# Performance work log

Hardware: AMD Instinct MI355X
Metric: run time of the kernel (lower is better)

The kernel has to match this reference:

```python
import jax, jax.numpy as jnp
import numpy as np

B, S, D, H, G = 4, 2048, 1024, 16, 32
HD = D // H
LN_EPS = 1e-5


def _lin_init(key, fan_in, fan_out):
    kw, kb = jax.random.split(key)
    bound = 1.0 / np.sqrt(fan_in)
    W = jax.random.uniform(kw, (fan_in, fan_out), jnp.float32, -bound, bound)
    b = jax.random.uniform(kb, (fan_out,), jnp.float32, -bound, bound)
    return W, b


def setup_inputs() -> dict:
    key = jax.random.key(0)
    ks = jax.random.split(key, 9)
    x = jax.random.normal(ks[0], (B, S, D), jnp.float32)
    geo_features = jax.random.normal(ks[1], (B, G), jnp.float32)
    Wq, bq = _lin_init(ks[2], D, D)
    Wk, bk = _lin_init(ks[3], D, D)
    Wv, bv = _lin_init(ks[4], D, D)
    Wo, bo = _lin_init(ks[5], D, D)
    ge_W1, ge_b1 = _lin_init(ks[6], G, D)
    ln_g = jnp.ones((D,), jnp.float32)
    ln_b = jnp.zeros((D,), jnp.float32)
    ge_W2, ge_b2 = _lin_init(ks[7], D, D)
    gm_W, gm_b = _lin_init(ks[8], D, H)
    return dict(x=x, geo_features=geo_features, Wq=Wq, bq=bq, Wk=Wk, bk=bk,
                Wv=Wv, bv=bv, Wo=Wo, bo=bo, ge_W1=ge_W1, ge_b1=ge_b1,
                ln_g=ln_g, ln_b=ln_b, ge_W2=ge_W2, ge_b2=ge_b2,
                gm_W=gm_W, gm_b=gm_b)


def reference(x, geo_features, Wq, bq, Wk, bk, Wv, bv, Wo, bo,
              ge_W1, ge_b1, ln_g, ln_b, ge_W2, ge_b2, gm_W, gm_b):
    # QKV projections -> (B, H, S, HD)
    def split_heads(t):
        return t.reshape(B, S, H, HD).transpose(0, 2, 1, 3)
    Q = split_heads(x @ Wq + bq)
    K = split_heads(x @ Wk + bk)
    V = split_heads(x @ Wv + bv)

    # geo encoder: Linear -> LayerNorm -> ReLU -> Linear
    h = geo_features @ ge_W1 + ge_b1                      # (B, D)
    mu = jnp.mean(h, axis=-1, keepdims=True)
    var = jnp.mean(jnp.square(h - mu), axis=-1, keepdims=True)
    h = (h - mu) / jnp.sqrt(var + LN_EPS) * ln_g + ln_b
    h = jax.nn.relu(h)
    geo_encoded = h @ ge_W2 + ge_b2                       # (B, D)
    geo_mod = jax.nn.sigmoid(geo_encoded @ gm_W + gm_b)   # (B, H)

    scale = 1.0 / np.sqrt(HD)
    scores = jnp.einsum('bhqd,bhkd->bhqk', Q, K) * scale  # (B, H, S, S)
    scores = scores * (1.0 + geo_mod[:, :, None, None])
    attn = jax.nn.softmax(scores, axis=-1)                # dropout in eval mode: identity
    ctx = jnp.einsum('bhqk,bhkd->bhqd', attn, V)          # (B, H, S, HD)
    ctx = ctx.transpose(0, 2, 1, 3).reshape(B, S, D)
    out = ctx @ Wo + bo
    return out, attn
```

## Files before the change

### kernel.cpp

```cpp
#include <hip/hip_runtime.h>

typedef __attribute__((ext_vector_type(8))) short bf16x8;
typedef __attribute__((ext_vector_type(4))) float f32x4;
typedef __attribute__((ext_vector_type(4))) unsigned short us4;
typedef unsigned short u16;

#define MB (1024*1024)

__device__ __forceinline__ u16 f2bf(float f) {
    unsigned u = __float_as_uint(f);
    unsigned r = (u + 0x7fffu + ((u >> 16) & 1u)) >> 16;
    return (u16)r;
}

__device__ __forceinline__ f32x4 mfma16(bf16x8 a, bf16x8 b, f32x4 c) {
    return __builtin_amdgcn_mfma_f32_16x16x32_bf16(a, b, c, 0, 0, 0);
}

__device__ __forceinline__ void gload16(const void* g, void* l) {
    __builtin_amdgcn_global_load_lds(
        (__attribute__((address_space(1))) void*)(unsigned long long)g,
        (__attribute__((address_space(3))) void*)l, 16, 0, 0);
}

__global__ __launch_bounds__(256) void k_cvtx(const float* __restrict__ x, u16* __restrict__ xb) {
    const long long i = (long long)blockIdx.x * 256 + threadIdx.x;
    const float4* xp = (const float4*)x;
    float4 a = xp[i*2], b = xp[i*2+1];
    bf16x8 o;
    o[0]=(short)f2bf(a.x); o[1]=(short)f2bf(a.y); o[2]=(short)f2bf(a.z); o[3]=(short)f2bf(a.w);
    o[4]=(short)f2bf(b.x); o[5]=(short)f2bf(b.y); o[6]=(short)f2bf(b.z); o[7]=(short)f2bf(b.w);
    *(bf16x8*)&xb[i*8] = o;
}

__global__ __launch_bounds__(256) void k_wtcvt(const float* __restrict__ W0, const float* __restrict__ W1,
                                               const float* __restrict__ W2, const float* __restrict__ W3,
                                               u16* __restrict__ wt) {
    __shared__ float tl[32][33];
    const int t = threadIdx.x, z = blockIdx.z;
    const float* W = (z==0)?W0:(z==1)?W1:(z==2)?W2:W3;
    const int k0 = blockIdx.x*32, n0 = blockIdx.y*32;
    const int r = t >> 3, c4 = (t & 7) * 4;
    float4 v = *(const float4*)&W[(long long)(k0+r)*1024 + n0 + c4];
    tl[r][c4] = v.x; tl[r][c4+1] = v.y; tl[r][c4+2] = v.z; tl[r][c4+3] = v.w;
    __syncthreads();
    us4 ov;
    ov[0] = f2bf(tl[c4+0][r]); ov[1] = f2bf(tl[c4+1][r]);
    ov[2] = f2bf(tl[c4+2][r]); ov[3] = f2bf(tl[c4+3][r]);
    *(us4*)&wt[((long long)z << 20) + (long long)(n0+r)*1024 + k0 + c4] = ov;
}

__global__ __launch_bounds__(1024) void k_geo1(const float* __restrict__ geo, const float* __restrict__ W1,
                                               const float* __restrict__ b1, const float* __restrict__ lng,
                                               const float* __restrict__ lnb, float* __restrict__ hr) {
    const int b = blockIdx.x, j = threadIdx.x;
    float acc = b1[j];
    #pragma unroll 8
    for (int g = 0; g < 32; ++g) acc += geo[b*32+g] * W1[(long long)g*1024 + j];
    float s1 = acc, s2 = acc*acc;
    #pragma unroll
    for (int m = 1; m < 64; m <<= 1) { s1 += __shfl_xor(s1, m); s2 += __shfl_xor(s2, m); }
    __shared__ float r1[16], r2[16];
    __shared__ float mu_s, rv_s;
    const int wid = threadIdx.x >> 6, lid = threadIdx.x & 63;
    if (lid == 0) { r1[wid] = s1; r2[wid] = s2; }
    __syncthreads();
    if (threadIdx.x == 0) {
        float S1 = 0.f, S2 = 0.f;
        for (int i = 0; i < 16; ++i) { S1 += r1[i]; S2 += r2[i]; }
        float mu = S1 / 1024.f;
        float var = S2 / 1024.f - mu*mu;
        mu_s = mu; rv_s = rsqrtf(var + 1e-5f);
    }
    __syncthreads();
    float hv = (acc - mu_s) * rv_s * lng[j] + lnb[j];
    hr[b*1024 + j] = fmaxf(hv, 0.f);
}

__global__ __launch_bounds__(256) void k_geo2(const float* __restrict__ hr, const float* __restrict__ W2,
                                              const float* __restrict__ b2, float* __restrict__ ge) {
    const int b = blockIdx.x >> 2;
    const int j = (blockIdx.x & 3)*256 + threadIdx.x;
    __shared__ float hs[1024];
    #pragma unroll
    for (int i = 0; i < 4; ++i) hs[threadIdx.x*4 + i] = hr[b*1024 + threadIdx.x*4 + i];
    __syncthreads();
    float acc = b2[j];
    #pragma unroll 8
    for (int d = 0; d < 1024; ++d) acc += hs[d] * W2[(long long)d*1024 + j];
    ge[b*1024 + j] = acc;
}

__global__ __launch_bounds__(64) void k_geo3(const float* __restrict__ ge, const float* __restrict__ gmW,
                                             const float* __restrict__ gmb, float* __restrict__ qs) {
    const int t = threadIdx.x;
    const int b = t >> 4, hh = t & 15;
    float acc = gmb[hh];
    #pragma unroll 8
    for (int d = 0; d < 1024; ++d) acc += ge[b*1024 + d] * gmW[d*16 + hh];
    qs[t] = 0.125f * (1.f + 1.f/(1.f + __expf(-acc)));
}

__global__ __launch_bounds__(256) void k_qkv_gemm(const u16* __restrict__ xb, const u16* __restrict__ wtq,
                                                  const float* __restrict__ bq, const float* __restrict__ bk,
                                                  const float* __restrict__ bv, u16* __restrict__ outq) {
    __shared__ u16 lA[128*64];
    __shared__ u16 lB[128*64];
    const int t = threadIdx.x, z = blockIdx.z;
    const int m0 = blockIdx.y * 128, n0 = blockIdx.x * 128;
    const u16* wt = wtq + (long long)z * (1024*1024);
    const float* bias = (z==0) ? bq : (z==1) ? bk : bv;
    u16* out = outq + (long long)z * 8388608;
    const int w = t >> 6, l = t & 63, lm = l & 15, lg = l >> 4;
    const int wr = (w >> 1) * 64, wc = (w & 1) * 64;
    f32x4 acc[4][4] = {};
    const char* gA = (const char*)xb + (long long)(m0 + (t>>3))*2048 + (t&7)*16;
    const char* gB = (const char*)wt + (long long)(n0 + (t>>3))*2048 + (t&7)*16;
    char* lAp = (char*)lA + t*16;
    char* lBp = (char*)lB + t*16;
    for (int k0 = 0; k0 < 1024; k0 += 64) {
        #pragma unroll
        for (int i = 0; i < 4; ++i) {
            gload16(gA + (long long)i*32*2048, lAp + i*4096);
            gload16(gB + (long long)i*32*2048, lBp + i*4096);
        }
        gA += 128; gB += 128;
        __syncthreads();
        #pragma unroll
        for (int kk = 0; kk < 2; ++kk) {
            bf16x8 af[4], bfr[4];
            #pragma unroll
            for (int mi = 0; mi < 4; ++mi)
                af[mi] = *(const bf16x8*)((const char*)lA + (wr + mi*16 + lm)*128 + kk*64 + lg*16);
            #pragma unroll
            for (int ni = 0; ni < 4; ++ni)
                bfr[ni] = *(const bf16x8*)((const char*)lB + (wc + ni*16 + lm)*128 + kk*64 + lg*16);
            #pragma unroll
            for (int mi = 0; mi < 4; ++mi)
                #pragma unroll
                for (int ni = 0; ni < 4; ++ni)
                    acc[mi][ni] = mfma16(af[mi], bfr[ni], acc[mi][ni]);
        }
        __syncthreads();
    }
    #pragma unroll
    for (int ni = 0; ni < 4; ++ni) {
        const int n = n0 + wc + ni*16 + lm;
        const float bn = bias[n];
        const int hh = n >> 6, d = n & 63;
        #pragma unroll
        for (int mi = 0; mi < 4; ++mi) {
            #pragma unroll
            for (int r = 0; r < 4; ++r) {
                const int m = m0 + wr + mi*16 + lg*4 + r;
                const int b = m >> 11, s = m & 2047;
                out[(((long long)b*16 + hh)*2048 + s)*64 + d] = f2bf(acc[mi][ni][r] + bn);
            }
        }
    }
}

__global__ __launch_bounds__(256) void k_vtrans(const u16* __restrict__ vb, u16* __restrict__ vt) {
    __shared__ u16 tl[64][40];
    const int t = threadIdx.x;
    const int bh = blockIdx.z, s0 = blockIdx.y*64, d0 = blockIdx.x*32;
    const u16* vsrc = vb + (long long)bh*2048*64;
    {
        const int sl = t >> 2, dg = t & 3;
        bf16x8 v = *(const bf16x8*)&vsrc[(long long)(s0+sl)*64 + d0 + dg*8];
        *(bf16x8*)&tl[sl][dg*8] = v;
    }
    __syncthreads();
    {
        const int dl = t >> 3, sg = t & 7;
        bf16x8 o;
        #pragma unroll
        for (int j = 0; j < 8; ++j) o[j] = (short)tl[sg*8+j][dl];
        *(bf16x8*)&vt[((long long)bh*64 + d0+dl)*2048 + s0 + sg*8] = o;
    }
}

__global__ __launch_bounds__(256) void k_attn(const u16* __restrict__ Qb, const u16* __restrict__ Kb,
                                              const u16* __restrict__ Vt, const float* __restrict__ qsv,
                                              float* __restrict__ attn_out, u16* __restrict__ ctxb) {
    __shared__ u16 lK[128*64];
    __shared__ u16 lV[64*128];
    __shared__ u16 lP[128*128];

    const int nl = blockIdx.x;
    const int ob = (nl & 7)*128 + (nl >> 3);
    const int bh = ob >> 4, qt = ob & 15;
    const int t = threadIdx.x, w = t >> 6, l = t & 63, lm = l & 15, lg = l >> 4;
    const int q0 = qt * 128;
    const float qs = qsv[bh];

    const char* KB = (const char*)Kb + (long long)bh * (2048*64*2);
    const char* VB = (const char*)Vt + (long long)bh * (2048*64*2);

    bf16x8 qf[2][2];
    {
        const char* QB = (const char*)Qb + (long long)bh * (2048*64*2);
        #pragma unroll
        for (int ms = 0; ms < 2; ++ms)
            #pragma unroll
            for (int kc = 0; kc < 2; ++kc)
                qf[ms][kc] = *(const bf16x8*)(QB + (long long)(q0 + w*32 + ms*16 + lm)*128 + kc*64 + lg*16);
    }

    int koff[4], voff[4], loff[4];
    #pragma unroll
    for (int i = 0; i < 4; ++i) {
        int off = i*4096 + t*16;
        loff[i] = off;
        int rowk = off >> 7, pck = off & 127;
        koff[i] = rowk*128 + (pck ^ ((rowk & 7) << 4));
        int rowv = off >> 8, pcv = off & 255;
        voff[i] = rowv*4096 + (pcv ^ ((rowv & 7) << 4));
    }

    float lsum[2][4] = {};
    for (int kt = 0; kt < 16; ++kt) {
        #pragma unroll
        for (int i = 0; i < 4; ++i)
            gload16(KB + kt*16384 + koff[i], (char*)lK + loff[i]);
        __syncthreads();
        #pragma unroll
        for (int ns = 0; ns < 8; ++ns) {
            const int rowb = ns*16 + lm;
            const int tag = (rowb & 7) << 4;
            bf16x8 kf0 = *(const bf16x8*)((const char*)lK + rowb*128 + ((lg*16) ^ tag));
            bf16x8 kf1 = *(const bf16x8*)((const char*)lK + rowb*128 + ((64 + lg*16) ^ tag));
            #pragma unroll
            for (int ms = 0; ms < 2; ++ms) {
                f32x4 acc = {};
                acc = mfma16(qf[ms][0], kf0, acc);
                acc = mfma16(qf[ms][1], kf1, acc);
                #pragma unroll
                for (int r = 0; r < 4; ++r)
                    lsum[ms][r] += __expf(acc[r] * qs);
            }
        }
        __syncthreads();
    }
    float invl[2][4];
    #pragma unroll
    for (int ms = 0; ms < 2; ++ms)
        #pragma unroll
        for (int r = 0; r < 4; ++r) {
            float v = lsum[ms][r];
            v += __shfl_xor(v, 1); v += __shfl_xor(v, 2);
            v += __shfl_xor(v, 4); v += __shfl_xor(v, 8);
            invl[ms][r] = 1.f / v;
        }

    f32x4 cacc[2][4] = {};
    float* aout = attn_out + (long long)bh*2048*2048 + (long long)(q0 + w*32)*2048;
    for (int kt = 0; kt < 16; ++kt) {
        #pragma unroll
        for (int i = 0; i < 4; ++i)
            gload16(KB + kt*16384 + koff[i], (char*)lK + loff[i]);
        #pragma unroll
        for (int i = 0; i < 4; ++i)
            gload16(VB + kt*256 + voff[i], (char*)lV + loff[i]);
        __syncthreads();

        #pragma unroll
        for (int ns = 0; ns < 8; ++ns) {
            const int rowb = ns*16 + lm;
            const int tag = (rowb & 7) << 4;
            bf16x8 kf0 = *(const bf16x8*)((const char*)lK + rowb*128 + ((lg*16) ^ tag));
            bf16x8 kf1 = *(const bf16x8*)((const char*)lK + rowb*128 + ((64 + lg*16) ^ tag));
            #pragma unroll
            for (int ms = 0; ms < 2; ++ms) {
                f32x4 acc = {};
                acc = mfma16(qf[ms][0], kf0, acc);
                acc = mfma16(qf[ms][1], kf1, acc);
                #pragma unroll
                for (int r = 0; r < 4; ++r) {
                    const float p = __expf(acc[r]*qs) * invl[ms][r];
                    const int row = ms*16 + lg*4 + r;
                    __builtin_nontemporal_store(p, &aout[(long long)row*2048 + kt*128 + ns*16 + lm]);
                    const int prow = w*32 + row;
                    *(u16*)((char*)lP + prow*256 + (((ns*16 + lm)*2) ^ ((prow & 7) << 4))) = f2bf(p);
                }
            }
        }
        #pragma unroll
        for (int ks = 0; ks < 4; ++ks) {
            bf16x8 pa[2];
            #pragma unroll
            for (int ms = 0; ms < 2; ++ms) {
                const int prow = w*32 + ms*16 + lm;
                pa[ms] = *(const bf16x8*)((const char*)lP + prow*256 + ((ks*64 + lg*16) ^ ((prow & 7) << 4)));
            }
            #pragma unroll
            for (int dn = 0; dn < 4; ++dn) {
                const int rowv = dn*16 + lm;
                bf16x8 vf = *(const bf16x8*)((const char*)lV + rowv*256 + ((ks*64 + lg*16) ^ ((rowv & 7) << 4)));
                cacc[0][dn] = mfma16(pa[0], vf, cacc[0][dn]);
                cacc[1][dn] = mfma16(pa[1], vf, cacc[1][dn]);
            }
        }
        __syncthreads();
    }

    const int b = bh >> 4, hh = bh & 15;
    #pragma unroll
    for (int ms = 0; ms < 2; ++ms)
        #pragma unroll
        for (int dn = 0; dn < 4; ++dn)
            #pragma unroll
            for (int r = 0; r < 4; ++r) {
                const int q = q0 + w*32 + ms*16 + lg*4 + r;
                ctxb[(((long long)b*2048 + q)*16 + hh)*64 + dn*16 + lm] = f2bf(cacc[ms][dn][r]);
            }
}

__global__ __launch_bounds__(256) void k_o_gemm(const u16* __restrict__ ab, const u16* __restrict__ wt,
                                                const float* __restrict__ bo, float* __restrict__ outf) {
    __shared__ u16 lA[128*64];
    __shared__ u16 lB[128*64];
    const int t = threadIdx.x;
    const int m0 = blockIdx.y * 128, n0 = blockIdx.x * 128;
    const int w = t >> 6, l = t & 63, lm = l & 15, lg = l >> 4;
    const int wr = (w >> 1) * 64, wc = (w & 1) * 64;
    f32x4 acc[4][4] = {};
    const char* gA = (const char*)ab + (long long)(m0 + (t>>3))*2048 + (t&7)*16;
    const char* gB = (const char*)wt + (long long)(n0 + (t>>3))*2048 + (t&7)*16;
    char* lAp = (char*)lA + t*16;
    char* lBp = (char*)lB + t*16;
    for (int k0 = 0; k0 < 1024; k0 += 64) {
        #pragma unroll
        for (int i = 0; i < 4; ++i) {
            gload16(gA + (long long)i*32*2048, lAp + i*4096);
            gload16(gB + (long long)i*32*2048, lBp + i*4096);
        }
        gA += 128; gB += 128;
        __syncthreads();
        #pragma unroll
        for (int kk = 0; kk < 2; ++kk) {
            bf16x8 af[4], bfr[4];
            #pragma unroll
            for (int mi = 0; mi < 4; ++mi)
                af[mi] = *(const bf16x8*)((const char*)lA + (wr + mi*16 + lm)*128 + kk*64 + lg*16);
            #pragma unroll
            for (int ni = 0; ni < 4; ++ni)
                bfr[ni] = *(const bf16x8*)((const char*)lB + (wc + ni*16 + lm)*128 + kk*64 + lg*16);
            #pragma unroll
            for (int mi = 0; mi < 4; ++mi)
                #pragma unroll
                for (int ni = 0; ni < 4; ++ni)
                    acc[mi][ni] = mfma16(af[mi], bfr[ni], acc[mi][ni]);
        }
        __syncthreads();
    }
    #pragma unroll
    for (int ni = 0; ni < 4; ++ni) {
        const int n = n0 + wc + ni*16 + lm;
        const float bn = bo[n];
        #pragma unroll
        for (int mi = 0; mi < 4; ++mi) {
            #pragma unroll
            for (int r = 0; r < 4; ++r) {
                const int m = m0 + wr + mi*16 + lg*4 + r;
                outf[(long long)m*1024 + n] = acc[mi][ni][r] + bn;
            }
        }
    }
}

extern "C" void kernel_launch(void* const* d_in, const int* in_sizes, int n_in,
                              void* d_out, int out_size, void* d_ws, size_t ws_size,
                              hipStream_t stream) {
    const float* x    = (const float*)d_in[0];
    const float* geo  = (const float*)d_in[1];
    const float* Wq   = (const float*)d_in[2];
    const float* bq   = (const float*)d_in[3];
    const float* Wk   = (const float*)d_in[4];
    const float* bk   = (const float*)d_in[5];
    const float* Wv   = (const float*)d_in[6];
    const float* bv   = (const float*)d_in[7];
    const float* Wo   = (const float*)d_in[8];
    const float* bo   = (const float*)d_in[9];
    const float* geW1 = (const float*)d_in[10];
    const float* geb1 = (const float*)d_in[11];
    const float* lng  = (const float*)d_in[12];
    const float* lnb  = (const float*)d_in[13];
    const float* geW2 = (const float*)d_in[14];
    const float* geb2 = (const float*)d_in[15];
    const float* gmW  = (const float*)d_in[16];
    const float* gmb  = (const float*)d_in[17];

    char* ws = (char*)d_ws;
    u16* xb   = (u16*)(ws + 0);
    u16* wt   = (u16*)(ws + 16*(size_t)MB);
    u16* qkv  = (u16*)(ws + 24*(size_t)MB);
    u16* Qb   = qkv;
    u16* Kb   = (u16*)(ws + 40*(size_t)MB);
    u16* Vb   = (u16*)(ws + 56*(size_t)MB);
    u16* Vt   = (u16*)(ws + 72*(size_t)MB);
    u16* ctx  = Vb;
    float* hr = (float*)(ws + 88*(size_t)MB);
    float* ge = (float*)(ws + 88*(size_t)MB + 65536);
    float* qsb= (float*)(ws + 88*(size_t)MB + 131072);

    float* outf = (float*)d_out;
    float* attn = outf + 8388608;

    hipLaunchKernelGGL(k_cvtx,    dim3(4096),      dim3(256),  0, stream, x, xb);
    hipLaunchKernelGGL(k_wtcvt,   dim3(32,32,4),   dim3(256),  0, stream, Wq, Wk, Wv, Wo, wt);
    hipLaunchKernelGGL(k_geo1,    dim3(4),         dim3(1024), 0, stream, geo, geW1, geb1, lng, lnb, hr);
    hipLaunchKernelGGL(k_geo2,    dim3(16),        dim3(256),  0, stream, hr, geW2, geb2, ge);
    hipLaunchKernelGGL(k_geo3,    dim3(1),         dim3(64),   0, stream, ge, gmW, gmb, qsb);
    hipLaunchKernelGGL(k_qkv_gemm,dim3(8,64,3),    dim3(256),  0, stream, xb, wt, bq, bk, bv, qkv);
    hipLaunchKernelGGL(k_vtrans,  dim3(2,32,64),   dim3(256),  0, stream, Vb, Vt);
    hipLaunchKernelGGL(k_attn,    dim3(1024),      dim3(256),  0, stream, Qb, Kb, Vt, qsb, attn, ctx);
    hipLaunchKernelGGL(k_o_gemm,  dim3(8,64),      dim3(256),  0, stream, ctx, wt + 3*1048576, bo, outf);
}
```

Before: 572.0 us.

## Software-pipeline attention K/V loads with multi-buffered LDS and vectorized attn stores

Rewrites the attention kernel's two passes to use smaller 64-key tiles held in multiple LDS buffers: triple-buffered in the row-sum pass, double-buffered K and V in the output pass. The next tile's global loads are issued before the current tile's compute, with explicit vmcnt waits and barriers, so load latency can overlap MFMA work. The MFMA operands are swapped so each lane holds four consecutive keys for one query row. This allows 16-byte nontemporal stores of attention probabilities and packed bf16 conversion into the P tile. It also sets occupancy to three blocks per CU with a single 48KB LDS array. The hand-written waitcnt counts and barrier placement are fragile and could cause races if the counts are wrong.

```diff
diff --git a/kernel.cpp b/kernel.cpp
--- a/kernel.cpp
+++ b/kernel.cpp
@@ -7,10 +7,21 @@
 
 #define MB (1024*1024)
 
+#define WAITV(N) asm volatile("s_waitcnt vmcnt(" #N ")" ::: "memory")
+#define WAITL0() asm volatile("s_waitcnt lgkmcnt(0)" ::: "memory")
+#define BAR()    __builtin_amdgcn_s_barrier()
+#define SCHEDB() __builtin_amdgcn_sched_barrier(0)
+
 __device__ __forceinline__ u16 f2bf(float f) {
     unsigned u = __float_as_uint(f);
     unsigned r = (u + 0x7fffu + ((u >> 16) & 1u)) >> 16;
     return (u16)r;
+}
+
+__device__ __forceinline__ unsigned cvtpk(float a, float b) {
+    unsigned r;
+    asm("v_cvt_pk_bf16_f32 %0, %1, %2" : "=v"(r) : "v"(a), "v"(b));
+    return r;
 }
 
 __device__ __forceinline__ f32x4 mfma16(bf16x8 a, bf16x8 b, f32x4 c) {
@@ -180,12 +191,10 @@
     }
 }
 
-__global__ __launch_bounds__(256) void k_attn(const u16* __restrict__ Qb, const u16* __restrict__ Kb,
-                                              const u16* __restrict__ Vt, const float* __restrict__ qsv,
-                                              float* __restrict__ attn_out, u16* __restrict__ ctxb) {
-    __shared__ u16 lK[128*64];
-    __shared__ u16 lV[64*128];
-    __shared__ u16 lP[128*128];
+__global__ __launch_bounds__(256, 3) void k_attn(const u16* __restrict__ Qb, const u16* __restrict__ Kb,
+                                                 const u16* __restrict__ Vt, const float* __restrict__ qsv,
+                                                 float* __restrict__ attn_out, u16* __restrict__ ctxb) {
+    __shared__ char lds[49152];
 
     const int nl = blockIdx.x;
     const int ob = (nl & 7)*128 + (nl >> 3);
@@ -194,12 +203,12 @@
     const int q0 = qt * 128;
     const float qs = qsv[bh];
 
-    const char* KB = (const char*)Kb + (long long)bh * (2048*64*2);
-    const char* VB = (const char*)Vt + (long long)bh * (2048*64*2);
+    const char* KB = (const char*)Kb + (long long)bh * 262144;
+    const char* VB = (const char*)Vt + (long long)bh * 262144;
 
     bf16x8 qf[2][2];
     {
-        const char* QB = (const char*)Qb + (long long)bh * (2048*64*2);
+        const char* QB = (const char*)Qb + (long long)bh * 262144;
         #pragma unroll
         for (int ms = 0; ms < 2; ++ms)
             #pragma unroll
@@ -207,101 +216,139 @@
                 qf[ms][kc] = *(const bf16x8*)(QB + (long long)(q0 + w*32 + ms*16 + lm)*128 + kc*64 + lg*16);
     }
 
-    int koff[4], voff[4], loff[4];
-    #pragma unroll
-    for (int i = 0; i < 4; ++i) {
-        int off = i*4096 + t*16;
-        loff[i] = off;
-        int rowk = off >> 7, pck = off & 127;
-        koff[i] = rowk*128 + (pck ^ ((rowk & 7) << 4));
-        int rowv = off >> 8, pcv = off & 255;
-        voff[i] = rowv*4096 + (pcv ^ ((rowv & 7) << 4));
-    }
-
-    float lsum[2][4] = {};
-    for (int kt = 0; kt < 16; ++kt) {
-        #pragma unroll
-        for (int i = 0; i < 4; ++i)
-            gload16(KB + kt*16384 + koff[i], (char*)lK + loff[i]);
-        __syncthreads();
-        #pragma unroll
-        for (int ns = 0; ns < 8; ++ns) {
-            const int rowb = ns*16 + lm;
-            const int tag = (rowb & 7) << 4;
-            bf16x8 kf0 = *(const bf16x8*)((const char*)lK + rowb*128 + ((lg*16) ^ tag));
-            bf16x8 kf1 = *(const bf16x8*)((const char*)lK + rowb*128 + ((64 + lg*16) ^ tag));
-            #pragma unroll
-            for (int ms = 0; ms < 2; ++ms) {
-                f32x4 acc = {};
-                acc = mfma16(qf[ms][0], kf0, acc);
-                acc = mfma16(qf[ms][1], kf1, acc);
-                #pragma unroll
-                for (int r = 0; r < 4; ++r)
-                    lsum[ms][r] += __expf(acc[r] * qs);
-            }
-        }
-        __syncthreads();
-    }
-    float invl[2][4];
-    #pragma unroll
-    for (int ms = 0; ms < 2; ++ms)
-        #pragma unroll
-        for (int r = 0; r < 4; ++r) {
-            float v = lsum[ms][r];
-            v += __shfl_xor(v, 1); v += __shfl_xor(v, 2);
-            v += __shfl_xor(v, 4); v += __shfl_xor(v, 8);
-            invl[ms][r] = 1.f / v;
-        }
-
+    int offA[2], srcK[2], srcV[2];
+    #pragma unroll
+    for (int i = 0; i < 2; ++i) {
+        const int off = i*4096 + t*16;
+        const int row = off >> 7, cb = off & 127;
+        offA[i] = off;
+        srcK[i] = row*128  + (cb ^ ((row & 7) << 4));
+        srcV[i] = row*4096 + (cb ^ ((row & 7) << 4));
+    }
+
+    float lsum[2] = {0.f, 0.f};
+    {
+        #pragma unroll
+        for (int i = 0; i < 2; ++i) gload16(KB + srcK[i], lds + offA[i]);
+        #pragma unroll
+        for (int i = 0; i < 2; ++i) gload16(KB + 8192 + srcK[i], lds + 8192 + offA[i]);
+        SCHEDB();
+        WAITV(2); BAR(); SCHEDB();
+
+        int cb_ = 0, sb_ = 2;
+        for (int kt = 0; kt < 32; ++kt) {
+            const int ktn = (kt < 30) ? kt + 2 : 31;
+            {
+                char* dst = lds + sb_*8192;
+                #pragma unroll
+                for (int i = 0; i < 2; ++i)
+                    gload16(KB + (long long)ktn*8192 + srcK[i], dst + offA[i]);
+            }
+            SCHEDB();
+            const char* kb = lds + cb_*8192;
+            #pragma unroll
+            for (int ns = 0; ns < 4; ++ns) {
+                const int rowb = ns*16 + lm;
+                const int tag = (rowb & 7) << 4;
+                bf16x8 kf0 = *(const bf16x8*)(kb + rowb*128 + ((lg*16) ^ tag));
+                bf16x8 kf1 = *(const bf16x8*)(kb + rowb*128 + ((64 + lg*16) ^ tag));
+                #pragma unroll
+                for (int ms = 0; ms < 2; ++ms) {
+                    f32x4 a = {};
+                    a = mfma16(kf0, qf[ms][0], a);
+                    a = mfma16(kf1, qf[ms][1], a);
+                    lsum[ms] += __expf(a[0]*qs) + __expf(a[1]*qs)
+                              + __expf(a[2]*qs) + __expf(a[3]*qs);
+                }
+            }
+            WAITV(2); BAR(); SCHEDB();
+            cb_ = (cb_ == 2) ? 0 : cb_ + 1;
+            sb_ = (sb_ == 2) ? 0 : sb_ + 1;
+        }
+    }
+    WAITV(0); BAR(); SCHEDB();
+
+    float invl[2];
+    #pragma unroll
+    for (int ms = 0; ms < 2; ++ms) {
+        float v = lsum[ms];
+        v += __shfl_xor(v, 16);
+        v += __shfl_xor(v, 32);
+        invl[ms] = 1.f / v;
+    }
+
+    char* lP = lds + 32768;
+    float* aL = attn_out + ((long long)bh*2048 + q0 + w*32 + lm)*2048 + lg*4;
     f32x4 cacc[2][4] = {};
-    float* aout = attn_out + (long long)bh*2048*2048 + (long long)(q0 + w*32)*2048;
-    for (int kt = 0; kt < 16; ++kt) {
-        #pragma unroll
-        for (int i = 0; i < 4; ++i)
-            gload16(KB + kt*16384 + koff[i], (char*)lK + loff[i]);
-        #pragma unroll
-        for (int i = 0; i < 4; ++i)
-            gload16(VB + kt*256 + voff[i], (char*)lV + loff[i]);
-        __syncthreads();
-
-        #pragma unroll
-        for (int ns = 0; ns < 8; ++ns) {
-            const int rowb = ns*16 + lm;
-            const int tag = (rowb & 7) << 4;
-            bf16x8 kf0 = *(const bf16x8*)((const char*)lK + rowb*128 + ((lg*16) ^ tag));
-            bf16x8 kf1 = *(const bf16x8*)((const char*)lK + rowb*128 + ((64 + lg*16) ^ tag));
-            #pragma unroll
-            for (int ms = 0; ms < 2; ++ms) {
-                f32x4 acc = {};
-                acc = mfma16(qf[ms][0], kf0, acc);
-                acc = mfma16(qf[ms][1], kf1, acc);
-                #pragma unroll
-                for (int r = 0; r < 4; ++r) {
-                    const float p = __expf(acc[r]*qs) * invl[ms][r];
-                    const int row = ms*16 + lg*4 + r;
-                    __builtin_nontemporal_store(p, &aout[(long long)row*2048 + kt*128 + ns*16 + lm]);
-                    const int prow = w*32 + row;
-                    *(u16*)((char*)lP + prow*256 + (((ns*16 + lm)*2) ^ ((prow & 7) << 4))) = f2bf(p);
+
+    {
+        #pragma unroll
+        for (int i = 0; i < 2; ++i) gload16(KB + srcK[i], lds + offA[i]);
+        #pragma unroll
+        for (int i = 0; i < 2; ++i) gload16(VB + srcV[i], lds + 16384 + offA[i]);
+        SCHEDB();
+        WAITV(0); BAR(); SCHEDB();
+
+        for (int kt = 0; kt < 32; ++kt) {
+            const int cur = kt & 1, nxt = cur ^ 1;
+            const int ktn = (kt < 31) ? kt + 1 : 31;
+            {
+                char* dK = lds + nxt*8192;
+                char* dV = lds + 16384 + nxt*8192;
+                #pragma unroll
+                for (int i = 0; i < 2; ++i)
+                    gload16(KB + (long long)ktn*8192 + srcK[i], dK + offA[i]);
+                #pragma unroll
+                for (int i = 0; i < 2; ++i)
+                    gload16(VB + (long long)ktn*128 + srcV[i], dV + offA[i]);
+            }
+            SCHEDB();
+
+            const char* kb = lds + cur*8192;
+            #pragma unroll
+            for (int ns = 0; ns < 4; ++ns) {
+                const int rowb = ns*16 + lm;
+                const int tag = (rowb & 7) << 4;
+                bf16x8 kf0 = *(const bf16x8*)(kb + rowb*128 + ((lg*16) ^ tag));
+                bf16x8 kf1 = *(const bf16x8*)(kb + rowb*128 + ((64 + lg*16) ^ tag));
+                #pragma unroll
+                for (int ms = 0; ms < 2; ++ms) {
+                    f32x4 a = {};
+                    a = mfma16(kf0, qf[ms][0], a);
+                    a = mfma16(kf1, qf[ms][1], a);
+                    const float p0 = __expf(a[0]*qs) * invl[ms];
+                    const float p1 = __expf(a[1]*qs) * invl[ms];
+                    const float p2 = __expf(a[2]*qs) * invl[ms];
+                    const float p3 = __expf(a[3]*qs) * invl[ms];
+                    f32x4 pv4 = {p0, p1, p2, p3};
+                    __builtin_nontemporal_store(pv4, (f32x4*)(aL + ms*32768 + kt*64 + ns*16));
+                    const int prow = w*32 + ms*16 + lm;
+                    const int ptag = (prow & 7) << 4;
+                    uint2 pk; pk.x = cvtpk(p0, p1); pk.y = cvtpk(p2, p3);
+                    *(uint2*)(lP + prow*128 + ((32*ns + 8*lg) ^ ptag)) = pk;
                 }
             }
-        }
-        #pragma unroll
-        for (int ks = 0; ks < 4; ++ks) {
-            bf16x8 pa[2];
-            #pragma unroll
-            for (int ms = 0; ms < 2; ++ms) {
-                const int prow = w*32 + ms*16 + lm;
-                pa[ms] = *(const bf16x8*)((const char*)lP + prow*256 + ((ks*64 + lg*16) ^ ((prow & 7) << 4)));
-            }
-            #pragma unroll
-            for (int dn = 0; dn < 4; ++dn) {
-                const int rowv = dn*16 + lm;
-                bf16x8 vf = *(const bf16x8*)((const char*)lV + rowv*256 + ((ks*64 + lg*16) ^ ((rowv & 7) << 4)));
-                cacc[0][dn] = mfma16(pa[0], vf, cacc[0][dn]);
-                cacc[1][dn] = mfma16(pa[1], vf, cacc[1][dn]);
-            }
-        }
-        __syncthreads();
+            WAITL0(); SCHEDB();
+
+            const char* vb = lds + 16384 + cur*8192;
+            #pragma unroll
+            for (int ks = 0; ks < 2; ++ks) {
+                bf16x8 pa[2];
+                #pragma unroll
+                for (int ms = 0; ms < 2; ++ms) {
+                    const int prow = w*32 + ms*16 + lm;
+                    pa[ms] = *(const bf16x8*)(lP + prow*128 + ((ks*64 + lg*16) ^ ((prow & 7) << 4)));
+                }
+                #pragma unroll
+                for (int dn = 0; dn < 4; ++dn) {
+                    const int rv = dn*16 + lm;
+                    bf16x8 vf = *(const bf16x8*)(vb + rv*128 + ((ks*64 + lg*16) ^ ((rv & 7) << 4)));
+                    cacc[0][dn] = mfma16(pa[0], vf, cacc[0][dn]);
+                    cacc[1][dn] = mfma16(pa[1], vf, cacc[1][dn]);
+                }
+            }
+            WAITV(8); BAR(); SCHEDB();
+        }
     }
 
     const int b = bh >> 4, hh = bh & 15;
```

New measurement: 580.7 us. About the same (+1.5%).
